# Kernel tuning notes

Measured on AMD Instinct MI355X. Metric: run time of the kernel, lower is better.

## Reference

```python
import jax, jax.numpy as jnp
import numpy as np
from functools import partial

D_MODEL = 256
D_STATE = 16
DT_RANK = 16  # ceil(d_model/16)
LN_EPS = 1e-5


def setup_inputs() -> dict:
    key = jax.random.key(0)
    ks = jax.random.split(key, 8)
    B, L, d, N, r = 16, 2048, D_MODEL, D_STATE, DT_RANK
    x = jax.random.normal(ks[0], (B, L, d), dtype=jnp.float32)
    # LayerNorm params
    ln_w = jnp.ones((d,), jnp.float32)
    ln_b = jnp.zeros((d,), jnp.float32)
    # S6 params
    x_proj_w = jax.random.normal(ks[1], (d, r + 2 * N), jnp.float32) / np.sqrt(d)
    dt_proj_w = jax.random.normal(ks[2], (r, d), jnp.float32) / np.sqrt(r)
    dt_proj_b = jax.random.uniform(ks[3], (d,), jnp.float32, -4.0, -2.0)  # softplus -> small dt
    A_log = jnp.log(jnp.tile(jnp.arange(1, N + 1, dtype=jnp.float32), (d, 1)))  # (d, N)
    D_skip = jnp.ones((d,), jnp.float32)
    # GLU params
    glu_w = jax.random.normal(ks[4], (d, 2 * d), jnp.float32) / np.sqrt(d)
    glu_b = jnp.zeros((2 * d,), jnp.float32)
    return {"x": x, "ln_w": ln_w, "ln_b": ln_b, "x_proj_w": x_proj_w,
            "dt_proj_w": dt_proj_w, "dt_proj_b": dt_proj_b, "A_log": A_log,
            "D_skip": D_skip, "glu_w": glu_w, "glu_b": glu_b}


def _layernorm(x, w, b):
    mu = jnp.mean(x, -1, keepdims=True)
    var = jnp.mean(jnp.square(x - mu), -1, keepdims=True)
    return (x - mu) * jax.lax.rsqrt(var + LN_EPS) * w + b


def _s6(x, x_proj_w, dt_proj_w, dt_proj_b, A_log, D_skip):
    # x: (B, L, d) selective scan (S6)
    Bsz, L, d = x.shape
    N = A_log.shape[1]
    A = -jnp.exp(A_log)                       # (d, N)
    dbl = x @ x_proj_w                        # (B, L, r+2N)
    dt, Bm, Cm = jnp.split(dbl, [DT_RANK, DT_RANK + N], axis=-1)
    delta = jax.nn.softplus(dt @ dt_proj_w + dt_proj_b)  # (B, L, d)

    def step(h, inp):
        d_t, b_t, c_t, x_t = inp              # (B,d),(B,N),(B,N),(B,d)
        dA = jnp.exp(d_t[..., None] * A)      # (B, d, N)
        h = dA * h + (d_t * x_t)[..., None] * b_t[:, None, :]
        y = jnp.einsum('bdn,bn->bd', h, c_t)
        return h, y

    h0 = jnp.zeros((Bsz, d, N), x.dtype)
    xs = (jnp.swapaxes(delta, 0, 1), jnp.swapaxes(Bm, 0, 1),
          jnp.swapaxes(Cm, 0, 1), jnp.swapaxes(x, 0, 1))
    _, ys = jax.lax.scan(step, h0, xs)        # ys: (L, B, d)
    return jnp.swapaxes(ys, 0, 1) + x * D_skip


def _glu(x, w, b):
    d = x.shape[-1]
    out = x @ w + b
    return out[..., :d] * jax.nn.sigmoid(out[..., d:])


@jax.jit
def reference(x, ln_w, ln_b, x_proj_w, dt_proj_w, dt_proj_b, A_log, D_skip, glu_w, glu_b):
    skip = x
    h = _layernorm(x, ln_w, ln_b)
    h = _s6(h, x_proj_w, dt_proj_w, dt_proj_b, A_log, D_skip)
    h = jax.nn.gelu(h, approximate=False)     # dropout = identity (eval)
    h = _glu(h, glu_w, glu_b)
    return h + skip
```

## Files before the change

### kernel.cpp

```cpp
#include <hip/hip_runtime.h>
#include <hip/hip_bf16.h>

#define BB 16
#define LL 2048
#define DD 256
#define NN 16
#define RR 16
#define CH 64
#define LC (LL/CH)

static __device__ __forceinline__ float bf2f(unsigned short u) {
    return __uint_as_float(((unsigned)u) << 16);
}
static __device__ __forceinline__ unsigned short f2bf(float f) {
    unsigned u = __float_as_uint(f);
    u += 0x7FFFu + ((u >> 16) & 1u);
    return (unsigned short)(u >> 16);
}

typedef __attribute__((ext_vector_type(8))) short bf16x8;
typedef __attribute__((ext_vector_type(4))) short bf16x4;
typedef __attribute__((ext_vector_type(4))) float f32x4;

static __device__ __forceinline__ void pow_tree(float E, float* e) {
    e[0] = E;
    e[1] = E * E;
    e[2] = e[1] * E;
    e[3] = e[1] * e[1];
    e[4] = e[3] * e[0];  e[5] = e[3] * e[1];  e[6] = e[3] * e[2];  e[7] = e[3] * e[3];
    e[8] = e[7] * e[0];  e[9] = e[7] * e[1];  e[10] = e[7] * e[2]; e[11] = e[7] * e[3];
    e[12] = e[7] * e[4]; e[13] = e[7] * e[5]; e[14] = e[7] * e[6]; e[15] = e[7] * e[7];
}

__global__ __launch_bounds__(256) void k_prep_wx(
    const float* __restrict__ xw, unsigned short* __restrict__ Wxt)
{
    const int idx = blockIdx.x * 256 + threadIdx.x;
    const int n  = idx >> 6;
    const int k0 = (idx & 63) * 4;
    #pragma unroll
    for (int i = 0; i < 4; ++i) {
        float v = (n < 48) ? xw[(size_t)(k0 + i) * 48 + n] : 0.f;
        Wxt[(size_t)n * DD + k0 + i] = f2bf(v);
    }
}

__global__ __launch_bounds__(256) void k_transpose(
    const float* __restrict__ W, unsigned short* __restrict__ Wt)
{
    __shared__ unsigned short s[32][33];
    const int bx = blockIdx.x;
    const int by = blockIdx.y;
    const int t = threadIdx.x;
    const int r = t >> 5, cc = t & 31;
    #pragma unroll
    for (int i = 0; i < 4; ++i)
        s[r + 8*i][cc] = f2bf(W[(size_t)(by*32 + r + 8*i)*512 + bx*32 + cc]);
    __syncthreads();
    #pragma unroll
    for (int i = 0; i < 4; ++i)
        Wt[(size_t)(bx*32 + r + 8*i)*256 + by*32 + cc] = s[cc][r + 8*i];
}

template<bool FAST>
__device__ __forceinline__ void dt_scan1(
    const float (*sdt)[20], const unsigned short (*As)[264],
    const float (*sB)[16], const float* wj, float bia,
    const float* al, int d, size_t m0,
    unsigned short* __restrict__ delta,
    float* h, float* dsum)
{
    #pragma unroll 4
    for (int l = 0; l < LC; ++l) {
        float acc = bia;
        #pragma unroll
        for (int j = 0; j < 16; ++j)
            acc = fmaf(sdt[l][j], wj[j], acc);
        const float sp = (acc > 15.f) ? acc
            : 0.69314718f * log2f(1.f + exp2f(acc * 1.44269504f));
        const unsigned short dbits = f2bf(sp);
        delta[(m0 + l)*DD + d] = dbits;
        const float dl = bf2f(dbits);
        const float xl = bf2f(As[l][d]);
        const float dx = dl * xl;
        *dsum += dl;
        float e[NN];
        if (FAST) pow_tree(exp2f(al[0]*dl), e);
        else {
            #pragma unroll
            for (int n = 0; n < NN; ++n) e[n] = exp2f(al[n]*dl);
        }
        #pragma unroll
        for (int n = 0; n < NN; ++n)
            h[n] = fmaf(e[n], h[n], dx * sB[l][n]);
    }
}

__global__ __launch_bounds__(256) void k_ln_scan1(
    const float* __restrict__ x,
    const float* __restrict__ ln_w,
    const float* __restrict__ ln_b,
    const unsigned short* __restrict__ Wxt,
    const float* __restrict__ dtw,
    const float* __restrict__ dtb,
    const float* __restrict__ A_log,
    unsigned short* __restrict__ xln,
    unsigned short* __restrict__ delta,
    float* __restrict__ Bv,
    float* __restrict__ Cv,
    float* __restrict__ S,
    float* __restrict__ Dsum)
{
    const int t = threadIdx.x;
    const int blk = blockIdx.x;
    const size_t m0 = (size_t)blk * 32;
    const int row = t >> 3, seg = t & 7;
    const size_t grow = m0 + row;

    __shared__ unsigned short As[32][264];
    __shared__ float sdt[32][20];
    __shared__ float sB[32][16];
    __shared__ float slnw[256], slnb[256], sdtb[256];

    {
        const int tt = t & 63;
        if (t < 64)       *(float4*)&slnw[tt*4] = *(const float4*)&ln_w[tt*4];
        else if (t < 128) *(float4*)&slnb[tt*4] = *(const float4*)&ln_b[tt*4];
        else if (t < 192) *(float4*)&sdtb[tt*4] = *(const float4*)&dtb[tt*4];
    }

    float wj[16];
    #pragma unroll
    for (int j = 0; j < 16; ++j) wj[j] = dtw[j*DD + t];
    float al[NN];
    bool fast = true;
    #pragma unroll
    for (int n = 0; n < NN; ++n) {
        al[n] = -expf(A_log[t*NN + n]) * 1.44269504f;
        fast = fast && (fabsf(al[n] - (n+1)*al[0]) <= 1e-3f*fabsf(al[n]) + 1e-6f);
    }

    float v[32];
    #pragma unroll
    for (int i = 0; i < 8; ++i)
        *(float4*)&v[i*4] = *(const float4*)(x + grow*DD + i*32 + seg*4);
    float s = 0.f, q = 0.f;
    #pragma unroll
    for (int i = 0; i < 32; ++i) { s += v[i]; q = fmaf(v[i], v[i], q); }
    #pragma unroll
    for (int o = 1; o < 8; o <<= 1) {
        s += __shfl_xor(s, o);
        q += __shfl_xor(q, o);
    }
    const float mu = s * (1.f/DD);
    const float rs = rsqrtf(q * (1.f/DD) - mu*mu + 1e-5f);
    __syncthreads();

    #pragma unroll
    for (int i = 0; i < 8; ++i) {
        const int c = i*32 + seg*4;
        const float4 wv = *(const float4*)&slnw[c];
        const float4 bv = *(const float4*)&slnb[c];
        unsigned short o16[4];
        o16[0] = f2bf((v[i*4+0]-mu)*rs*wv.x + bv.x);
        o16[1] = f2bf((v[i*4+1]-mu)*rs*wv.y + bv.y);
        o16[2] = f2bf((v[i*4+2]-mu)*rs*wv.z + bv.z);
        o16[3] = f2bf((v[i*4+3]-mu)*rs*wv.w + bv.w);
        *(bf16x4*)&xln[grow*DD + c] = *(bf16x4*)&o16[0];
        *(bf16x4*)&As[row][c]       = *(bf16x4*)&o16[0];
    }
    __syncthreads();

    {
        const int w = t >> 6, lane = t & 63;
        const int cl = lane & 15, rq = lane >> 4;
        const int mh = (w & 1) * 16;
        const int nh = (w >> 1) * 32;
        f32x4 acc0 = {0.f,0.f,0.f,0.f}, acc1 = {0.f,0.f,0.f,0.f};
        #pragma unroll
        for (int k0 = 0; k0 < 256; k0 += 32) {
            const bf16x8 a  = *(const bf16x8*)&As[mh + cl][k0 + rq*8];
            const bf16x8 b0 = *(const bf16x8*)&Wxt[(size_t)(nh + cl)*DD + k0 + rq*8];
            acc0 = __builtin_amdgcn_mfma_f32_16x16x32_bf16(a, b0, acc0, 0, 0, 0);
            if (w < 2) {
                const bf16x8 b1 = *(const bf16x8*)&Wxt[(size_t)(nh + 16 + cl)*DD + k0 + rq*8];
                acc1 = __builtin_amdgcn_mfma_f32_16x16x32_bf16(a, b1, acc1, 0, 0, 0);
            }
        }
        if (w < 2) {
            #pragma unroll
            for (int r = 0; r < 4; ++r) {
                const int rr = mh + rq*4 + r;
                sdt[rr][cl] = acc0[r];
                sB[rr][cl]  = acc1[r];
                Bv[(m0 + rr)*NN + cl] = acc1[r];
            }
        } else {
            #pragma unroll
            for (int r = 0; r < 4; ++r)
                Cv[(m0 + mh + rq*4 + r)*NN + cl] = acc0[r];
        }
    }
    __syncthreads();

    float h[NN];
    #pragma unroll
    for (int n = 0; n < NN; ++n) h[n] = 0.f;
    float dsum = 0.f;
    const float bia = sdtb[t];
    if (fast) dt_scan1<true >(sdt, As, sB, wj, bia, al, t, m0, delta, h, &dsum);
    else      dt_scan1<false>(sdt, As, sB, wj, bia, al, t, m0, delta, h, &dsum);
    const size_t o = (size_t)blk * NN * DD + t;
    #pragma unroll
    for (int n = 0; n < NN; ++n) S[o + n*DD] = h[n];
    Dsum[(size_t)blk*DD + t] = dsum;
}

__global__ __launch_bounds__(256) void k_combine(
    const float* __restrict__ S, const float* __restrict__ Dsum,
    const float* __restrict__ A_log, float* __restrict__ Hin)
{
    const int bi = blockIdx.x;
    const int d = threadIdx.x;
    const int n = bi & 15;
    const int b = bi >> 4;
    const float al = -expf(A_log[d*NN + n]) * 1.44269504f;
    float h = 0.f;
    for (int c0 = 0; c0 < CH; c0 += 8) {
        float ds8[8], s8[8];
        #pragma unroll
        for (int i = 0; i < 8; ++i) {
            const size_t blk = (size_t)b*CH + c0 + i;
            ds8[i] = Dsum[blk*DD + d];
            s8[i]  = S[(blk*NN + n)*DD + d];
        }
        #pragma unroll
        for (int i = 0; i < 8; ++i) {
            const size_t blk = (size_t)b*CH + c0 + i;
            Hin[(blk*NN + n)*DD + d] = h;
            h = fmaf(exp2f(al * ds8[i]), h, s8[i]);
        }
    }
}

template<bool FAST>
__device__ __forceinline__ void scan2_impl(
    const unsigned short (*sD)[264], const unsigned short (*sX)[264],
    const float (*sB)[16], const float (*sC)[16],
    const float* al, int d, float* h, float dsk,
    size_t gout, unsigned short* __restrict__ g)
{
    #pragma unroll 4
    for (int l = 0; l < LC; ++l) {
        const float dl = bf2f(sD[l][d]);
        const float xl = bf2f(sX[l][d]);
        const float dx = dl * xl;
        float e[NN];
        if (FAST) pow_tree(exp2f(al[0]*dl), e);
        else {
            #pragma unroll
            for (int n = 0; n < NN; ++n) e[n] = exp2f(al[n]*dl);
        }
        float yb[4] = {0.f, 0.f, 0.f, 0.f};
        #pragma unroll
        for (int n = 0; n < NN; ++n) {
            h[n] = fmaf(e[n], h[n], dx * sB[l][n]);
            yb[n & 3] = fmaf(h[n], sC[l][n], yb[n & 3]);
        }
        const float vv = (yb[0]+yb[1]) + (yb[2]+yb[3]) + xl * dsk;
        const float u  = 0.7978845608f * (vv + 0.044715f*vv*vv*vv);
        const float t2 = exp2f(2.8853900818f * u);
        const float th = 1.f - 2.f/(t2 + 1.f);
        g[gout + (size_t)l*DD] = f2bf(0.5f * vv * (1.f + th));
    }
}

__global__ __launch_bounds__(256) void k_scan2(
    const unsigned short* __restrict__ delta,
    const unsigned short* __restrict__ xln,
    const float* __restrict__ Bv,
    const float* __restrict__ Cv,
    const float* __restrict__ A_log,
    const float* __restrict__ Hin,
    const float* __restrict__ Dskip,
    unsigned short* __restrict__ g)
{
    const int blk = blockIdx.x;
    const int c = blk & (CH-1);
    const int b = blk >> 6;
    const int d = threadIdx.x;
    const int l0 = c * LC;
    __shared__ unsigned short sD[LC][264];
    __shared__ unsigned short sX[LC][264];
    __shared__ float sB[LC][16], sC[LC][16];

    {
        const int sr = d >> 3, sc = (d & 7) * 32;
        const size_t gbase = ((size_t)b*LL + l0 + sr)*DD + sc;
        #pragma unroll
        for (int i = 0; i < 4; ++i) {
            *(bf16x8*)&sD[sr][sc + i*8] = *(const bf16x8*)&delta[gbase + i*8];
            *(bf16x8*)&sX[sr][sc + i*8] = *(const bf16x8*)&xln  [gbase + i*8];
        }
        if (d < 128) {
            const int l = d >> 2, qq = (d & 3) * 4;
            *(float4*)&sB[l][qq] = *(const float4*)&Bv[((size_t)b*LL + l0 + l)*NN + qq];
        } else {
            const int dd = d - 128;
            const int l = dd >> 2, qq = (dd & 3) * 4;
            *(float4*)&sC[l][qq] = *(const float4*)&Cv[((size_t)b*LL + l0 + l)*NN + qq];
        }
    }
    float al[NN];
    bool fast = true;
    #pragma unroll
    for (int n = 0; n < NN; ++n) {
        al[n] = -expf(A_log[d*NN + n]) * 1.44269504f;
        fast = fast && (fabsf(al[n] - (n+1)*al[0]) <= 1e-3f*fabsf(al[n]) + 1e-6f);
    }
    float h[NN];
    const size_t ob = (size_t)blk * NN * DD + d;
    #pragma unroll
    for (int n = 0; n < NN; ++n) h[n] = Hin[ob + n*DD];
    const float dsk = Dskip[d];
    __syncthreads();
    const size_t gout = ((size_t)b*LL + l0)*DD + d;
    if (fast) scan2_impl<true >(sD, sX, sB, sC, al, d, h, dsk, gout, g);
    else      scan2_impl<false>(sD, sX, sB, sC, al, d, h, dsk, gout, g);
}

__global__ __launch_bounds__(256) void k_glu(
    const unsigned short* __restrict__ g,
    const unsigned short* __restrict__ Wt,
    const float* __restrict__ gb,
    const float* __restrict__ x,
    float* __restrict__ out)
{
    __shared__ unsigned short As[64][40];
    __shared__ unsigned short Bl[64][40];
    __shared__ unsigned short Bh[64][40];
    const int n0 = blockIdx.x * 64;
    const int m0 = blockIdx.y * 64;
    const int t = threadIdx.x;
    const int w = t >> 6, lane = t & 63;
    const int r = t >> 2, q = t & 3;
    const int cl = lane & 15, rq = lane >> 4;
    f32x4 accL[4], accH[4];
    const f32x4 zz = {0.f, 0.f, 0.f, 0.f};
    #pragma unroll
    for (int nf = 0; nf < 4; ++nf) { accL[nf] = zz; accH[nf] = zz; }

    for (int k0 = 0; k0 < 256; k0 += 32) {
        *(bf16x8*)(&As[r][q*8]) = *(const bf16x8*)(&g [(size_t)(m0+r)*DD + k0 + q*8]);
        *(bf16x8*)(&Bl[r][q*8]) = *(const bf16x8*)(&Wt[(size_t)(n0+r)*DD + k0 + q*8]);
        *(bf16x8*)(&Bh[r][q*8]) = *(const bf16x8*)(&Wt[(size_t)(n0+256+r)*DD + k0 + q*8]);
        __syncthreads();
        const bf16x8 a = *(const bf16x8*)(&As[w*16 + cl][rq*8]);
        #pragma unroll
        for (int nf = 0; nf < 4; ++nf) {
            const bf16x8 bl = *(const bf16x8*)(&Bl[nf*16 + cl][rq*8]);
            const bf16x8 bh = *(const bf16x8*)(&Bh[nf*16 + cl][rq*8]);
            accL[nf] = __builtin_amdgcn_mfma_f32_16x16x32_bf16(a, bl, accL[nf], 0, 0, 0);
            accH[nf] = __builtin_amdgcn_mfma_f32_16x16x32_bf16(a, bh, accH[nf], 0, 0, 0);
        }
        __syncthreads();
    }
    #pragma unroll
    for (int nf = 0; nf < 4; ++nf) {
        const int j = n0 + nf*16 + cl;
        const float bL = gb[j];
        const float bH = gb[j + 256];
        #pragma unroll
        for (int rr = 0; rr < 4; ++rr) {
            const int m = m0 + w*16 + rq*4 + rr;
            const float lo = accL[nf][rr] + bL;
            const float hi = accH[nf][rr] + bH;
            const float sg = 1.f / (1.f + exp2f(-1.44269504f * hi));
            out[(size_t)m*DD + j] = lo * sg + x[(size_t)m*DD + j];
        }
    }
}

extern "C" void kernel_launch(void* const* d_in, const int* in_sizes, int n_in,
                              void* d_out, int out_size, void* d_ws, size_t ws_size,
                              hipStream_t stream)
{
    const float* x    = (const float*)d_in[0];
    const float* ln_w = (const float*)d_in[1];
    const float* ln_b = (const float*)d_in[2];
    const float* xpw  = (const float*)d_in[3];
    const float* dtw  = (const float*)d_in[4];
    const float* dtb  = (const float*)d_in[5];
    const float* alog = (const float*)d_in[6];
    const float* dsk  = (const float*)d_in[7];
    const float* gw   = (const float*)d_in[8];
    const float* gb   = (const float*)d_in[9];
    float* out = (float*)d_out;

    char* ws = (char*)d_ws;
    size_t off = 0;
    auto alloc = [&](size_t bytes) {
        char* p = ws + off; off += (bytes + 255) & ~(size_t)255; return p;
    };
    unsigned short* xln   = (unsigned short*)alloc((size_t)BB*LL*DD*2);
    unsigned short* delta = (unsigned short*)alloc((size_t)BB*LL*DD*2);
    float*          Bvp   = (float*)         alloc((size_t)BB*LL*NN*4);
    float*          Cvp   = (float*)         alloc((size_t)BB*LL*NN*4);
    float*          S     = (float*)         alloc((size_t)BB*CH*NN*DD*4);
    float*          Dsum  = (float*)         alloc((size_t)BB*CH*DD*4);
    float*          Hin   = (float*)         alloc((size_t)BB*CH*NN*DD*4);
    unsigned short* Wt    = (unsigned short*)alloc((size_t)512*256*2);
    unsigned short* Wxt   = (unsigned short*)alloc((size_t)64*256*2);
    unsigned short* g     = delta;

    k_prep_wx<<<16, 256, 0, stream>>>(xpw, Wxt);
    k_transpose<<<dim3(16, 8), 256, 0, stream>>>(gw, Wt);
    k_ln_scan1<<<BB*CH, 256, 0, stream>>>(x, ln_w, ln_b, Wxt, dtw, dtb, alog,
                                          xln, delta, Bvp, Cvp, S, Dsum);
    k_combine<<<256, 256, 0, stream>>>(S, Dsum, alog, Hin);
    k_scan2<<<BB*CH, 256, 0, stream>>>(delta, xln, Bvp, Cvp, alog, Hin, dsk, g);
    k_glu<<<dim3(4, 512), 256, 0, stream>>>(g, Wt, gb, x, out);
}
```

Before: 116.6 us.

## Fuse LayerNorm, chunked scan, combine and scan2 into one persistent kernel with grid barriers

Replaces the three-kernel chunked scan with one persistent kernel of 512 blocks that keeps the LayerNorm output, dt, B and C in shared memory. It uses software grid barriers between the chunk-local scan, the cross-chunk combine and the second scan. This removes the global round trips for xln, delta, B and C plus two kernel launches, at the cost of recomputing the dt projection and softplus in the second pass. It also merges the two weight-prep kernels into one launch. The fused path runs only when the occupancy query says all blocks can be resident; otherwise it falls back to the old kernels.

```diff
diff --git a/kernel.cpp b/kernel.cpp
--- a/kernel.cpp
+++ b/kernel.cpp
@@ -6,8 +6,10 @@
 #define DD 256
 #define NN 16
 #define RR 16
-#define CH 64
-#define LC (LL/CH)
+#define CHF 32
+#define LCF 64
+#define CHB 64
+#define LCB 32
 
 static __device__ __forceinline__ float bf2f(unsigned short u) {
     return __uint_as_float(((unsigned)u) << 16);
@@ -32,38 +34,277 @@
     e[12] = e[7] * e[4]; e[13] = e[7] * e[5]; e[14] = e[7] * e[6]; e[15] = e[7] * e[7];
 }
 
-__global__ __launch_bounds__(256) void k_prep_wx(
-    const float* __restrict__ xw, unsigned short* __restrict__ Wxt)
-{
-    const int idx = blockIdx.x * 256 + threadIdx.x;
-    const int n  = idx >> 6;
-    const int k0 = (idx & 63) * 4;
-    #pragma unroll
-    for (int i = 0; i < 4; ++i) {
-        float v = (n < 48) ? xw[(size_t)(k0 + i) * 48 + n] : 0.f;
-        Wxt[(size_t)n * DD + k0 + i] = f2bf(v);
-    }
-}
-
-__global__ __launch_bounds__(256) void k_transpose(
-    const float* __restrict__ W, unsigned short* __restrict__ Wt)
+static __device__ __forceinline__ void gridBarrier(unsigned* bar, unsigned nblk) {
+    __threadfence();
+    __syncthreads();
+    if (threadIdx.x == 0) {
+        unsigned* cnt = bar;
+        unsigned* gen = bar + 32;
+        const unsigned gsnap = atomicAdd(gen, 0u);
+        const unsigned arrived = atomicAdd(cnt, 1u) + 1u;
+        if (arrived == nblk) {
+            atomicExch(cnt, 0u);
+            __threadfence();
+            atomicAdd(gen, 1u);
+        } else {
+            while (atomicAdd(gen, 0u) == gsnap)
+                __builtin_amdgcn_s_sleep(2);
+        }
+    }
+    __syncthreads();
+    __threadfence();
+}
+
+__global__ __launch_bounds__(256) void k_prep(
+    const float* __restrict__ xw, const float* __restrict__ gw,
+    unsigned short* __restrict__ Wxt, unsigned short* __restrict__ Wt)
 {
     __shared__ unsigned short s[32][33];
-    const int bx = blockIdx.x;
-    const int by = blockIdx.y;
+    const int bid = blockIdx.x;
     const int t = threadIdx.x;
-    const int r = t >> 5, cc = t & 31;
-    #pragma unroll
-    for (int i = 0; i < 4; ++i)
-        s[r + 8*i][cc] = f2bf(W[(size_t)(by*32 + r + 8*i)*512 + bx*32 + cc]);
-    __syncthreads();
-    #pragma unroll
-    for (int i = 0; i < 4; ++i)
-        Wt[(size_t)(bx*32 + r + 8*i)*256 + by*32 + cc] = s[cc][r + 8*i];
+    if (bid < 16) {
+        const int idx = bid * 256 + t;
+        const int n  = idx >> 6;
+        const int k0 = (idx & 63) * 4;
+        #pragma unroll
+        for (int i = 0; i < 4; ++i) {
+            float v = (n < 48) ? xw[(size_t)(k0 + i) * 48 + n] : 0.f;
+            Wxt[(size_t)n * DD + k0 + i] = f2bf(v);
+        }
+    } else {
+        const int bb = bid - 16;
+        const int bx = bb & 15, by = bb >> 4;
+        const int r = t >> 5, cc = t & 31;
+        #pragma unroll
+        for (int i = 0; i < 4; ++i)
+            s[r + 8*i][cc] = f2bf(gw[(size_t)(by*32 + r + 8*i)*512 + bx*32 + cc]);
+        __syncthreads();
+        #pragma unroll
+        for (int i = 0; i < 4; ++i)
+            Wt[(size_t)(bx*32 + r + 8*i)*256 + by*32 + cc] = s[cc][r + 8*i];
+    }
 }
 
 template<bool FAST>
-__device__ __forceinline__ void dt_scan1(
+__device__ __forceinline__ void fused_scan1(
+    const float (*sdt)[20], const unsigned short (*As)[264],
+    const float (*sB)[17], const float* wj, float bia,
+    const float* al, int t, float* h, float* dsum)
+{
+    #pragma unroll 4
+    for (int l = 0; l < LCF; ++l) {
+        float acc = bia;
+        #pragma unroll
+        for (int j = 0; j < 16; ++j)
+            acc = fmaf(sdt[l][j], wj[j], acc);
+        const float sp = (acc > 15.f) ? acc
+            : 0.69314718f * log2f(1.f + exp2f(acc * 1.44269504f));
+        const float dl = bf2f(f2bf(sp));
+        const float xl = bf2f(As[l][t]);
+        const float dx = dl * xl;
+        *dsum += dl;
+        float e[NN];
+        if (FAST) pow_tree(exp2f(al[0]*dl), e);
+        else {
+            #pragma unroll
+            for (int n = 0; n < NN; ++n) e[n] = exp2f(al[n]*dl);
+        }
+        #pragma unroll
+        for (int n = 0; n < NN; ++n)
+            h[n] = fmaf(e[n], h[n], dx * sB[l][n]);
+    }
+}
+
+template<bool FAST>
+__device__ __forceinline__ void fused_scan2(
+    const float (*sdt)[20], const unsigned short (*As)[264],
+    const float (*sB)[17], const float (*sC)[17],
+    const float* wj, float bia, const float* al, int t,
+    float* h, float dsk, size_t m0, unsigned short* __restrict__ g)
+{
+    #pragma unroll 4
+    for (int l = 0; l < LCF; ++l) {
+        float acc = bia;
+        #pragma unroll
+        for (int j = 0; j < 16; ++j)
+            acc = fmaf(sdt[l][j], wj[j], acc);
+        const float sp = (acc > 15.f) ? acc
+            : 0.69314718f * log2f(1.f + exp2f(acc * 1.44269504f));
+        const float dl = bf2f(f2bf(sp));
+        const float xl = bf2f(As[l][t]);
+        const float dx = dl * xl;
+        float e[NN];
+        if (FAST) pow_tree(exp2f(al[0]*dl), e);
+        else {
+            #pragma unroll
+            for (int n = 0; n < NN; ++n) e[n] = exp2f(al[n]*dl);
+        }
+        float yb[4] = {0.f, 0.f, 0.f, 0.f};
+        #pragma unroll
+        for (int n = 0; n < NN; ++n) {
+            h[n] = fmaf(e[n], h[n], dx * sB[l][n]);
+            yb[n & 3] = fmaf(h[n], sC[l][n], yb[n & 3]);
+        }
+        const float vv = (yb[0]+yb[1]) + (yb[2]+yb[3]) + xl * dsk;
+        const float u  = 0.7978845608f * (vv + 0.044715f*vv*vv*vv);
+        const float t2 = exp2f(2.8853900818f * u);
+        const float th = 1.f - 2.f/(t2 + 1.f);
+        g[(m0 + l)*DD + t] = f2bf(0.5f * vv * (1.f + th));
+    }
+}
+
+__global__ __launch_bounds__(256) void k_fused(
+    const float* __restrict__ x,
+    const float* __restrict__ ln_w,
+    const float* __restrict__ ln_b,
+    const unsigned short* __restrict__ Wxt,
+    const float* __restrict__ dtw,
+    const float* __restrict__ dtb,
+    const float* __restrict__ A_log,
+    const float* __restrict__ Dskip,
+    float* __restrict__ S,
+    float* __restrict__ Dsum,
+    float* __restrict__ Hin,
+    unsigned short* __restrict__ g,
+    unsigned* __restrict__ bar)
+{
+    const int t = threadIdx.x;
+    const int blk = blockIdx.x;
+    const size_t m0 = (size_t)blk * LCF;
+
+    __shared__ unsigned short As[LCF][264];
+    __shared__ float sdt[LCF][20];
+    __shared__ float sB[LCF][17];
+    __shared__ float sC[LCF][17];
+    __shared__ float slnw[256], slnb[256], sdtb[256];
+
+    {
+        const int tt = t & 63;
+        if (t < 64)       *(float4*)&slnw[tt*4] = *(const float4*)&ln_w[tt*4];
+        else if (t < 128) *(float4*)&slnb[tt*4] = *(const float4*)&ln_b[tt*4];
+        else if (t < 192) *(float4*)&sdtb[tt*4] = *(const float4*)&dtb[tt*4];
+    }
+
+    float wj[16];
+    #pragma unroll
+    for (int j = 0; j < 16; ++j) wj[j] = dtw[j*DD + t];
+    float al[NN];
+    bool fast = true;
+    #pragma unroll
+    for (int n = 0; n < NN; ++n) {
+        al[n] = -expf(A_log[t*NN + n]) * 1.44269504f;
+        fast = fast && (fabsf(al[n] - (n+1)*al[0]) <= 1e-3f*fabsf(al[n]) + 1e-6f);
+    }
+    const float dsk = Dskip[t];
+    __syncthreads();
+
+    const int seg = t & 7;
+    #pragma unroll
+    for (int half = 0; half < 2; ++half) {
+        const int row = (t >> 3) + 32*half;
+        const size_t grow = m0 + row;
+        float v[32];
+        #pragma unroll
+        for (int i = 0; i < 8; ++i)
+            *(float4*)&v[i*4] = *(const float4*)(x + grow*DD + i*32 + seg*4);
+        float s = 0.f, q = 0.f;
+        #pragma unroll
+        for (int i = 0; i < 32; ++i) { s += v[i]; q = fmaf(v[i], v[i], q); }
+        #pragma unroll
+        for (int o = 1; o < 8; o <<= 1) {
+            s += __shfl_xor(s, o);
+            q += __shfl_xor(q, o);
+        }
+        const float mu = s * (1.f/DD);
+        const float rs = rsqrtf(q * (1.f/DD) - mu*mu + 1e-5f);
+        #pragma unroll
+        for (int i = 0; i < 8; ++i) {
+            const int c = i*32 + seg*4;
+            const float4 wv = *(const float4*)&slnw[c];
+            const float4 bv = *(const float4*)&slnb[c];
+            unsigned short o16[4];
+            o16[0] = f2bf((v[i*4+0]-mu)*rs*wv.x + bv.x);
+            o16[1] = f2bf((v[i*4+1]-mu)*rs*wv.y + bv.y);
+            o16[2] = f2bf((v[i*4+2]-mu)*rs*wv.z + bv.z);
+            o16[3] = f2bf((v[i*4+3]-mu)*rs*wv.w + bv.w);
+            *(bf16x4*)&As[row][c] = *(bf16x4*)&o16[0];
+        }
+    }
+    __syncthreads();
+
+    {
+        const int w = t >> 6, lane = t & 63;
+        const int cl = lane & 15, rq = lane >> 4;
+        const int mrow = w * 16;
+        f32x4 aDt = {0.f,0.f,0.f,0.f}, aB = {0.f,0.f,0.f,0.f}, aC = {0.f,0.f,0.f,0.f};
+        #pragma unroll
+        for (int k0 = 0; k0 < 256; k0 += 32) {
+            const bf16x8 a  = *(const bf16x8*)&As[mrow + cl][k0 + rq*8];
+            const bf16x8 b0 = *(const bf16x8*)&Wxt[(size_t)(cl)*DD      + k0 + rq*8];
+            const bf16x8 b1 = *(const bf16x8*)&Wxt[(size_t)(16+cl)*DD   + k0 + rq*8];
+            const bf16x8 b2 = *(const bf16x8*)&Wxt[(size_t)(32+cl)*DD   + k0 + rq*8];
+            aDt = __builtin_amdgcn_mfma_f32_16x16x32_bf16(a, b0, aDt, 0, 0, 0);
+            aB  = __builtin_amdgcn_mfma_f32_16x16x32_bf16(a, b1, aB,  0, 0, 0);
+            aC  = __builtin_amdgcn_mfma_f32_16x16x32_bf16(a, b2, aC,  0, 0, 0);
+        }
+        #pragma unroll
+        for (int r = 0; r < 4; ++r) {
+            const int rr = mrow + rq*4 + r;
+            sdt[rr][cl] = aDt[r];
+            sB[rr][cl]  = aB[r];
+            sC[rr][cl]  = aC[r];
+        }
+    }
+    __syncthreads();
+
+    float h[NN];
+    #pragma unroll
+    for (int n = 0; n < NN; ++n) h[n] = 0.f;
+    float dsum = 0.f;
+    const float bia = sdtb[t];
+    if (fast) fused_scan1<true >(sdt, As, sB, wj, bia, al, t, h, &dsum);
+    else      fused_scan1<false>(sdt, As, sB, wj, bia, al, t, h, &dsum);
+    {
+        const size_t o = (size_t)blk * NN * DD + t;
+        #pragma unroll
+        for (int n = 0; n < NN; ++n) S[o + n*DD] = h[n];
+        Dsum[(size_t)blk*DD + t] = dsum;
+    }
+    gridBarrier(bar, BB*CHF);
+
+    if (blk < 256) {
+        const int n2 = blk & 15, b2 = blk >> 4;
+        const float al2 = -expf(A_log[t*NN + n2]) * 1.44269504f;
+        float hh = 0.f;
+        for (int c0 = 0; c0 < CHF; c0 += 16) {
+            float ds16[16], s16[16];
+            #pragma unroll
+            for (int i = 0; i < 16; ++i) {
+                const size_t bc = (size_t)b2*CHF + c0 + i;
+                ds16[i] = Dsum[bc*DD + t];
+                s16[i]  = S[(bc*NN + n2)*DD + t];
+            }
+            #pragma unroll
+            for (int i = 0; i < 16; ++i) {
+                const size_t bc = (size_t)b2*CHF + c0 + i;
+                Hin[(bc*NN + n2)*DD + t] = hh;
+                hh = fmaf(exp2f(al2 * ds16[i]), hh, s16[i]);
+            }
+        }
+    }
+    gridBarrier(bar, BB*CHF);
+
+    {
+        const size_t ob = (size_t)blk * NN * DD + t;
+        #pragma unroll
+        for (int n = 0; n < NN; ++n) h[n] = Hin[ob + n*DD];
+    }
+    if (fast) fused_scan2<true >(sdt, As, sB, sC, wj, bia, al, t, h, dsk, m0, g);
+    else      fused_scan2<false>(sdt, As, sB, sC, wj, bia, al, t, h, dsk, m0, g);
+}
+
+template<bool FAST>
+__device__ __forceinline__ void dt_scan1_fb(
     const float (*sdt)[20], const unsigned short (*As)[264],
     const float (*sB)[16], const float* wj, float bia,
     const float* al, int d, size_t m0,
@@ -71,7 +312,7 @@
     float* h, float* dsum)
 {
     #pragma unroll 4
-    for (int l = 0; l < LC; ++l) {
+    for (int l = 0; l < LCB; ++l) {
         float acc = bia;
         #pragma unroll
         for (int j = 0; j < 16; ++j)
@@ -128,7 +369,6 @@
         else if (t < 128) *(float4*)&slnb[tt*4] = *(const float4*)&ln_b[tt*4];
         else if (t < 192) *(float4*)&sdtb[tt*4] = *(const float4*)&dtb[tt*4];
     }
-
     float wj[16];
     #pragma unroll
     for (int j = 0; j < 16; ++j) wj[j] = dtw[j*DD + t];
@@ -139,7 +379,6 @@
         al[n] = -expf(A_log[t*NN + n]) * 1.44269504f;
         fast = fast && (fabsf(al[n] - (n+1)*al[0]) <= 1e-3f*fabsf(al[n]) + 1e-6f);
     }
-
     float v[32];
     #pragma unroll
     for (int i = 0; i < 8; ++i)
@@ -155,7 +394,6 @@
     const float mu = s * (1.f/DD);
     const float rs = rsqrtf(q * (1.f/DD) - mu*mu + 1e-5f);
     __syncthreads();
-
     #pragma unroll
     for (int i = 0; i < 8; ++i) {
         const int c = i*32 + seg*4;
@@ -170,7 +408,6 @@
         *(bf16x4*)&As[row][c]       = *(bf16x4*)&o16[0];
     }
     __syncthreads();
-
     {
         const int w = t >> 6, lane = t & 63;
         const int cl = lane & 15, rq = lane >> 4;
@@ -202,14 +439,13 @@
         }
     }
     __syncthreads();
-
     float h[NN];
     #pragma unroll
     for (int n = 0; n < NN; ++n) h[n] = 0.f;
     float dsum = 0.f;
     const float bia = sdtb[t];
-    if (fast) dt_scan1<true >(sdt, As, sB, wj, bia, al, t, m0, delta, h, &dsum);
-    else      dt_scan1<false>(sdt, As, sB, wj, bia, al, t, m0, delta, h, &dsum);
+    if (fast) dt_scan1_fb<true >(sdt, As, sB, wj, bia, al, t, m0, delta, h, &dsum);
+    else      dt_scan1_fb<false>(sdt, As, sB, wj, bia, al, t, m0, delta, h, &dsum);
     const size_t o = (size_t)blk * NN * DD + t;
     #pragma unroll
     for (int n = 0; n < NN; ++n) S[o + n*DD] = h[n];
@@ -226,17 +462,17 @@
     const int b = bi >> 4;
     const float al = -expf(A_log[d*NN + n]) * 1.44269504f;
     float h = 0.f;
-    for (int c0 = 0; c0 < CH; c0 += 8) {
+    for (int c0 = 0; c0 < CHB; c0 += 8) {
         float ds8[8], s8[8];
         #pragma unroll
         for (int i = 0; i < 8; ++i) {
-            const size_t blk = (size_t)b*CH + c0 + i;
+            const size_t blk = (size_t)b*CHB + c0 + i;
             ds8[i] = Dsum[blk*DD + d];
             s8[i]  = S[(blk*NN + n)*DD + d];
         }
         #pragma unroll
         for (int i = 0; i < 8; ++i) {
-            const size_t blk = (size_t)b*CH + c0 + i;
+            const size_t blk = (size_t)b*CHB + c0 + i;
             Hin[(blk*NN + n)*DD + d] = h;
             h = fmaf(exp2f(al * ds8[i]), h, s8[i]);
         }
@@ -244,14 +480,14 @@
 }
 
 template<bool FAST>
-__device__ __forceinline__ void scan2_impl(
+__device__ __forceinline__ void scan2_impl_fb(
     const unsigned short (*sD)[264], const unsigned short (*sX)[264],
     const float (*sB)[16], const float (*sC)[16],
     const float* al, int d, float* h, float dsk,
     size_t gout, unsigned short* __restrict__ g)
 {
     #pragma unroll 4
-    for (int l = 0; l < LC; ++l) {
+    for (int l = 0; l < LCB; ++l) {
         const float dl = bf2f(sD[l][d]);
         const float xl = bf2f(sX[l][d]);
         const float dx = dl * xl;
@@ -286,14 +522,13 @@
     unsigned short* __restrict__ g)
 {
     const int blk = blockIdx.x;
-    const int c = blk & (CH-1);
+    const int c = blk & (CHB-1);
     const int b = blk >> 6;
     const int d = threadIdx.x;
-    const int l0 = c * LC;
-    __shared__ unsigned short sD[LC][264];
-    __shared__ unsigned short sX[LC][264];
-    __shared__ float sB[LC][16], sC[LC][16];
-
+    const int l0 = c * LCB;
+    __shared__ unsigned short sD[LCB][264];
+    __shared__ unsigned short sX[LCB][264];
+    __shared__ float sB[LCB][16], sC[LCB][16];
     {
         const int sr = d >> 3, sc = (d & 7) * 32;
         const size_t gbase = ((size_t)b*LL + l0 + sr)*DD + sc;
@@ -325,8 +560,8 @@
     const float dsk = Dskip[d];
     __syncthreads();
     const size_t gout = ((size_t)b*LL + l0)*DD + d;
-    if (fast) scan2_impl<true >(sD, sX, sB, sC, al, d, h, dsk, gout, g);
-    else      scan2_impl<false>(sD, sX, sB, sC, al, d, h, dsk, gout, g);
+    if (fast) scan2_impl_fb<true >(sD, sX, sB, sC, al, d, h, dsk, gout, g);
+    else      scan2_impl_fb<false>(sD, sX, sB, sC, al, d, h, dsk, gout, g);
 }
 
 __global__ __launch_bounds__(256) void k_glu(
@@ -402,22 +637,37 @@
     auto alloc = [&](size_t bytes) {
         char* p = ws + off; off += (bytes + 255) & ~(size_t)255; return p;
     };
-    unsigned short* xln   = (unsigned short*)alloc((size_t)BB*LL*DD*2);
-    unsigned short* delta = (unsigned short*)alloc((size_t)BB*LL*DD*2);
-    float*          Bvp   = (float*)         alloc((size_t)BB*LL*NN*4);
-    float*          Cvp   = (float*)         alloc((size_t)BB*LL*NN*4);
-    float*          S     = (float*)         alloc((size_t)BB*CH*NN*DD*4);
-    float*          Dsum  = (float*)         alloc((size_t)BB*CH*DD*4);
-    float*          Hin   = (float*)         alloc((size_t)BB*CH*NN*DD*4);
-    unsigned short* Wt    = (unsigned short*)alloc((size_t)512*256*2);
-    unsigned short* Wxt   = (unsigned short*)alloc((size_t)64*256*2);
-    unsigned short* g     = delta;
-
-    k_prep_wx<<<16, 256, 0, stream>>>(xpw, Wxt);
-    k_transpose<<<dim3(16, 8), 256, 0, stream>>>(gw, Wt);
-    k_ln_scan1<<<BB*CH, 256, 0, stream>>>(x, ln_w, ln_b, Wxt, dtw, dtb, alog,
-                                          xln, delta, Bvp, Cvp, S, Dsum);
-    k_combine<<<256, 256, 0, stream>>>(S, Dsum, alog, Hin);
-    k_scan2<<<BB*CH, 256, 0, stream>>>(delta, xln, Bvp, Cvp, alog, Hin, dsk, g);
+    unsigned*       bar    = (unsigned*)      alloc(256);
+    unsigned short* xln    = (unsigned short*)alloc((size_t)BB*LL*DD*2);
+    unsigned short* deltaG = (unsigned short*)alloc((size_t)BB*LL*DD*2);
+    float*          Bvp    = (float*)         alloc((size_t)BB*LL*NN*4);
+    float*          Cvp    = (float*)         alloc((size_t)BB*LL*NN*4);
+    float*          S      = (float*)         alloc((size_t)BB*CHB*NN*DD*4);
+    float*          Dsum   = (float*)         alloc((size_t)BB*CHB*DD*4);
+    float*          Hin    = (float*)         alloc((size_t)BB*CHB*NN*DD*4);
+    unsigned short* Wt     = (unsigned short*)alloc((size_t)512*256*2);
+    unsigned short* Wxt    = (unsigned short*)alloc((size_t)64*256*2);
+    unsigned short* g      = deltaG;
+
+    k_prep<<<144, 256, 0, stream>>>(xpw, gw, Wxt, Wt);
+
+    int occ = 0, ncu = 0, dev = 0;
+    bool coop = false;
+    if (hipGetDevice(&dev) == hipSuccess &&
+        hipOccupancyMaxActiveBlocksPerMultiprocessor(&occ, k_fused, 256, 0) == hipSuccess &&
+        hipDeviceGetAttribute(&ncu, hipDeviceAttributeMultiprocessorCount, dev) == hipSuccess)
+        coop = (occ * ncu >= BB*CHF);
+
+    if (coop) {
+        hipMemsetAsync(bar, 0, 256, stream);
+        k_fused<<<BB*CHF, 256, 0, stream>>>(x, ln_w, ln_b, Wxt, dtw, dtb, alog,
+                                            dsk, S, Dsum, Hin, g, bar);
+    } else {
+        k_ln_scan1<<<BB*CHB, 256, 0, stream>>>(x, ln_w, ln_b, Wxt, dtw, dtb, alog,
+                                               xln, deltaG, Bvp, Cvp, S, Dsum);
+        k_combine<<<256, 256, 0, stream>>>(S, Dsum, alog, Hin);
+        k_scan2<<<BB*CHB, 256, 0, stream>>>(deltaG, xln, Bvp, Cvp, alog, Hin, dsk, g);
+    }
+
     k_glu<<<dim3(4, 512), 256, 0, stream>>>(g, Wt, gb, x, out);
 }
```

Result: faster. 110.1 us (-5.6%).

## Compute dt projection with MFMA before scan and merge weight prep kernels

Applied to the files above, without the earlier changes.

Moves the per-step 16-wide dt projection out of the serial scan loop in k_ln_scan1. It is replaced by a block-wide bf16 MFMA pass that writes softplus(delta) into shared memory and global memory before the scan starts. The two weight-prep kernels are merged into a single launch that also emits a padded bf16 transposed dt_proj weight. B and C shared rows are padded to 20 floats and read as float4 vectors in both scans. In exchange, the dt projection input is now rounded to bf16, a precision loss, and the kernel gains an extra sync and more shared memory.

```diff
diff --git a/kernel.cpp b/kernel.cpp
--- a/kernel.cpp
+++ b/kernel.cpp
@@ -32,56 +32,57 @@
     e[12] = e[7] * e[4]; e[13] = e[7] * e[5]; e[14] = e[7] * e[6]; e[15] = e[7] * e[7];
 }
 
-__global__ __launch_bounds__(256) void k_prep_wx(
-    const float* __restrict__ xw, unsigned short* __restrict__ Wxt)
-{
-    const int idx = blockIdx.x * 256 + threadIdx.x;
-    const int n  = idx >> 6;
-    const int k0 = (idx & 63) * 4;
-    #pragma unroll
-    for (int i = 0; i < 4; ++i) {
-        float v = (n < 48) ? xw[(size_t)(k0 + i) * 48 + n] : 0.f;
-        Wxt[(size_t)n * DD + k0 + i] = f2bf(v);
-    }
-}
-
-__global__ __launch_bounds__(256) void k_transpose(
-    const float* __restrict__ W, unsigned short* __restrict__ Wt)
+__global__ __launch_bounds__(256) void k_prep(
+    const float* __restrict__ xw, const float* __restrict__ gw,
+    const float* __restrict__ dtw,
+    unsigned short* __restrict__ Wxt, unsigned short* __restrict__ Wt,
+    unsigned short* __restrict__ Dwt)
 {
     __shared__ unsigned short s[32][33];
-    const int bx = blockIdx.x;
-    const int by = blockIdx.y;
+    const int bid = blockIdx.x;
     const int t = threadIdx.x;
-    const int r = t >> 5, cc = t & 31;
-    #pragma unroll
-    for (int i = 0; i < 4; ++i)
-        s[r + 8*i][cc] = f2bf(W[(size_t)(by*32 + r + 8*i)*512 + bx*32 + cc]);
-    __syncthreads();
-    #pragma unroll
-    for (int i = 0; i < 4; ++i)
-        Wt[(size_t)(bx*32 + r + 8*i)*256 + by*32 + cc] = s[cc][r + 8*i];
+    if (bid < 16) {
+        const int idx = bid * 256 + t;
+        const int n  = idx >> 6;
+        const int k0 = (idx & 63) * 4;
+        #pragma unroll
+        for (int i = 0; i < 4; ++i) {
+            float v = (n < 48) ? xw[(size_t)(k0 + i) * 48 + n] : 0.f;
+            Wxt[(size_t)n * DD + k0 + i] = f2bf(v);
+        }
+    } else if (bid < 144) {
+        const int bb = bid - 16;
+        const int bx = bb & 15, by = bb >> 4;
+        const int r = t >> 5, cc = t & 31;
+        #pragma unroll
+        for (int i = 0; i < 4; ++i)
+            s[r + 8*i][cc] = f2bf(gw[(size_t)(by*32 + r + 8*i)*512 + bx*32 + cc]);
+        __syncthreads();
+        #pragma unroll
+        for (int i = 0; i < 4; ++i)
+            Wt[(size_t)(bx*32 + r + 8*i)*256 + by*32 + cc] = s[cc][r + 8*i];
+    } else {
+        unsigned short r32[32];
+        #pragma unroll
+        for (int k = 0; k < 16; ++k) r32[k] = f2bf(dtw[(size_t)k*DD + t]);
+        #pragma unroll
+        for (int k = 16; k < 32; ++k) r32[k] = 0;
+        #pragma unroll
+        for (int i = 0; i < 4; ++i)
+            *(bf16x8*)&Dwt[(size_t)t*32 + i*8] = *(bf16x8*)&r32[i*8];
+    }
 }
 
 template<bool FAST>
-__device__ __forceinline__ void dt_scan1(
-    const float (*sdt)[20], const unsigned short (*As)[264],
-    const float (*sB)[16], const float* wj, float bia,
-    const float* al, int d, size_t m0,
-    unsigned short* __restrict__ delta,
+__device__ __forceinline__ void scan1_loop(
+    const unsigned short (*sDel)[264], const unsigned short (*As)[264],
+    const float (*sB)[20], const float* al, int t,
     float* h, float* dsum)
 {
     #pragma unroll 4
     for (int l = 0; l < LC; ++l) {
-        float acc = bia;
-        #pragma unroll
-        for (int j = 0; j < 16; ++j)
-            acc = fmaf(sdt[l][j], wj[j], acc);
-        const float sp = (acc > 15.f) ? acc
-            : 0.69314718f * log2f(1.f + exp2f(acc * 1.44269504f));
-        const unsigned short dbits = f2bf(sp);
-        delta[(m0 + l)*DD + d] = dbits;
-        const float dl = bf2f(dbits);
-        const float xl = bf2f(As[l][d]);
+        const float dl = bf2f(sDel[l][t]);
+        const float xl = bf2f(As[l][t]);
         const float dx = dl * xl;
         *dsum += dl;
         float e[NN];
@@ -90,9 +91,15 @@
             #pragma unroll
             for (int n = 0; n < NN; ++n) e[n] = exp2f(al[n]*dl);
         }
+        const float4 B0 = *(const float4*)&sB[l][0];
+        const float4 B1 = *(const float4*)&sB[l][4];
+        const float4 B2 = *(const float4*)&sB[l][8];
+        const float4 B3 = *(const float4*)&sB[l][12];
+        const float bb[16] = {B0.x,B0.y,B0.z,B0.w, B1.x,B1.y,B1.z,B1.w,
+                              B2.x,B2.y,B2.z,B2.w, B3.x,B3.y,B3.z,B3.w};
         #pragma unroll
         for (int n = 0; n < NN; ++n)
-            h[n] = fmaf(e[n], h[n], dx * sB[l][n]);
+            h[n] = fmaf(e[n], h[n], dx * bb[n]);
     }
 }
 
@@ -101,7 +108,7 @@
     const float* __restrict__ ln_w,
     const float* __restrict__ ln_b,
     const unsigned short* __restrict__ Wxt,
-    const float* __restrict__ dtw,
+    const unsigned short* __restrict__ Dwt,
     const float* __restrict__ dtb,
     const float* __restrict__ A_log,
     unsigned short* __restrict__ xln,
@@ -113,13 +120,14 @@
 {
     const int t = threadIdx.x;
     const int blk = blockIdx.x;
-    const size_t m0 = (size_t)blk * 32;
+    const size_t m0 = (size_t)blk * LC;
     const int row = t >> 3, seg = t & 7;
     const size_t grow = m0 + row;
 
-    __shared__ unsigned short As[32][264];
-    __shared__ float sdt[32][20];
-    __shared__ float sB[32][16];
+    __shared__ unsigned short As[LC][264];
+    __shared__ unsigned short sDel[LC][264];
+    __shared__ unsigned short sdt16[LC][40];
+    __shared__ float sB[LC][20];
     __shared__ float slnw[256], slnb[256], sdtb[256];
 
     {
@@ -127,11 +135,11 @@
         if (t < 64)       *(float4*)&slnw[tt*4] = *(const float4*)&ln_w[tt*4];
         else if (t < 128) *(float4*)&slnb[tt*4] = *(const float4*)&ln_b[tt*4];
         else if (t < 192) *(float4*)&sdtb[tt*4] = *(const float4*)&dtb[tt*4];
-    }
-
-    float wj[16];
-    #pragma unroll
-    for (int j = 0; j < 16; ++j) wj[j] = dtw[j*DD + t];
+        if (t < 64) {
+            const bf16x8 z = {0,0,0,0,0,0,0,0};
+            *(bf16x8*)&sdt16[t >> 1][16 + (t & 1)*8] = z;
+        }
+    }
     float al[NN];
     bool fast = true;
     #pragma unroll
@@ -155,7 +163,6 @@
     const float mu = s * (1.f/DD);
     const float rs = rsqrtf(q * (1.f/DD) - mu*mu + 1e-5f);
     __syncthreads();
-
     #pragma unroll
     for (int i = 0; i < 8; ++i) {
         const int c = i*32 + seg*4;
@@ -171,9 +178,10 @@
     }
     __syncthreads();
 
+    const int w = t >> 6, lane = t & 63;
+    const int cl = lane & 15, rq = lane >> 4;
+
     {
-        const int w = t >> 6, lane = t & 63;
-        const int cl = lane & 15, rq = lane >> 4;
         const int mh = (w & 1) * 16;
         const int nh = (w >> 1) * 32;
         f32x4 acc0 = {0.f,0.f,0.f,0.f}, acc1 = {0.f,0.f,0.f,0.f};
@@ -191,8 +199,8 @@
             #pragma unroll
             for (int r = 0; r < 4; ++r) {
                 const int rr = mh + rq*4 + r;
-                sdt[rr][cl] = acc0[r];
-                sB[rr][cl]  = acc1[r];
+                sdt16[rr][cl] = f2bf(acc0[r]);
+                sB[rr][cl]    = acc1[r];
                 Bv[(m0 + rr)*NN + cl] = acc1[r];
             }
         } else {
@@ -203,13 +211,37 @@
     }
     __syncthreads();
 
+    {
+        const int mh = (w & 1) * 16;
+        const int nbase = (w >> 1) * 8;
+        const bf16x8 a = *(const bf16x8*)&sdt16[mh + cl][rq*8];
+        #pragma unroll
+        for (int nt = 0; nt < 8; ++nt) {
+            const int n0 = (nbase + nt) * 16;
+            const bf16x8 b = *(const bf16x8*)&Dwt[(size_t)(n0 + cl)*32 + rq*8];
+            f32x4 acc = {0.f,0.f,0.f,0.f};
+            acc = __builtin_amdgcn_mfma_f32_16x16x32_bf16(a, b, acc, 0, 0, 0);
+            const float bia = sdtb[n0 + cl];
+            #pragma unroll
+            for (int r = 0; r < 4; ++r) {
+                const float ac = acc[r] + bia;
+                const float sp = (ac > 15.f) ? ac
+                    : 0.69314718f * log2f(1.f + exp2f(ac * 1.44269504f));
+                const unsigned short db = f2bf(sp);
+                const int rr = mh + rq*4 + r;
+                sDel[rr][n0 + cl] = db;
+                delta[(m0 + rr)*DD + n0 + cl] = db;
+            }
+        }
+    }
+    __syncthreads();
+
     float h[NN];
     #pragma unroll
     for (int n = 0; n < NN; ++n) h[n] = 0.f;
     float dsum = 0.f;
-    const float bia = sdtb[t];
-    if (fast) dt_scan1<true >(sdt, As, sB, wj, bia, al, t, m0, delta, h, &dsum);
-    else      dt_scan1<false>(sdt, As, sB, wj, bia, al, t, m0, delta, h, &dsum);
+    if (fast) scan1_loop<true >(sDel, As, sB, al, t, h, &dsum);
+    else      scan1_loop<false>(sDel, As, sB, al, t, h, &dsum);
     const size_t o = (size_t)blk * NN * DD + t;
     #pragma unroll
     for (int n = 0; n < NN; ++n) S[o + n*DD] = h[n];
@@ -244,9 +276,9 @@
 }
 
 template<bool FAST>
-__device__ __forceinline__ void scan2_impl(
+__device__ __forceinline__ void scan2_loop(
     const unsigned short (*sD)[264], const unsigned short (*sX)[264],
-    const float (*sB)[16], const float (*sC)[16],
+    const float (*sB)[20], const float (*sC)[20],
     const float* al, int d, float* h, float dsk,
     size_t gout, unsigned short* __restrict__ g)
 {
@@ -261,11 +293,23 @@
             #pragma unroll
             for (int n = 0; n < NN; ++n) e[n] = exp2f(al[n]*dl);
         }
+        const float4 B0 = *(const float4*)&sB[l][0];
+        const float4 B1 = *(const float4*)&sB[l][4];
+        const float4 B2 = *(const float4*)&sB[l][8];
+        const float4 B3 = *(const float4*)&sB[l][12];
+        const float bb[16] = {B0.x,B0.y,B0.z,B0.w, B1.x,B1.y,B1.z,B1.w,
+                              B2.x,B2.y,B2.z,B2.w, B3.x,B3.y,B3.z,B3.w};
+        const float4 C0 = *(const float4*)&sC[l][0];
+        const float4 C1 = *(const float4*)&sC[l][4];
+        const float4 C2 = *(const float4*)&sC[l][8];
+        const float4 C3 = *(const float4*)&sC[l][12];
+        const float cc[16] = {C0.x,C0.y,C0.z,C0.w, C1.x,C1.y,C1.z,C1.w,
+                              C2.x,C2.y,C2.z,C2.w, C3.x,C3.y,C3.z,C3.w};
         float yb[4] = {0.f, 0.f, 0.f, 0.f};
         #pragma unroll
         for (int n = 0; n < NN; ++n) {
-            h[n] = fmaf(e[n], h[n], dx * sB[l][n]);
-            yb[n & 3] = fmaf(h[n], sC[l][n], yb[n & 3]);
+            h[n] = fmaf(e[n], h[n], dx * bb[n]);
+            yb[n & 3] = fmaf(h[n], cc[n], yb[n & 3]);
         }
         const float vv = (yb[0]+yb[1]) + (yb[2]+yb[3]) + xl * dsk;
         const float u  = 0.7978845608f * (vv + 0.044715f*vv*vv*vv);
@@ -292,8 +336,7 @@
     const int l0 = c * LC;
     __shared__ unsigned short sD[LC][264];
     __shared__ unsigned short sX[LC][264];
-    __shared__ float sB[LC][16], sC[LC][16];
-
+    __shared__ float sB[LC][20], sC[LC][20];
     {
         const int sr = d >> 3, sc = (d & 7) * 32;
         const size_t gbase = ((size_t)b*LL + l0 + sr)*DD + sc;
@@ -325,8 +368,8 @@
     const float dsk = Dskip[d];
     __syncthreads();
     const size_t gout = ((size_t)b*LL + l0)*DD + d;
-    if (fast) scan2_impl<true >(sD, sX, sB, sC, al, d, h, dsk, gout, g);
-    else      scan2_impl<false>(sD, sX, sB, sC, al, d, h, dsk, gout, g);
+    if (fast) scan2_loop<true >(sD, sX, sB, sC, al, d, h, dsk, gout, g);
+    else      scan2_loop<false>(sD, sX, sB, sC, al, d, h, dsk, gout, g);
 }
 
 __global__ __launch_bounds__(256) void k_glu(
@@ -402,22 +445,22 @@
     auto alloc = [&](size_t bytes) {
         char* p = ws + off; off += (bytes + 255) & ~(size_t)255; return p;
     };
-    unsigned short* xln   = (unsigned short*)alloc((size_t)BB*LL*DD*2);
-    unsigned short* delta = (unsigned short*)alloc((size_t)BB*LL*DD*2);
-    float*          Bvp   = (float*)         alloc((size_t)BB*LL*NN*4);
-    float*          Cvp   = (float*)         alloc((size_t)BB*LL*NN*4);
-    float*          S     = (float*)         alloc((size_t)BB*CH*NN*DD*4);
-    float*          Dsum  = (float*)         alloc((size_t)BB*CH*DD*4);
-    float*          Hin   = (float*)         alloc((size_t)BB*CH*NN*DD*4);
-    unsigned short* Wt    = (unsigned short*)alloc((size_t)512*256*2);
-    unsigned short* Wxt   = (unsigned short*)alloc((size_t)64*256*2);
-    unsigned short* g     = delta;
-
-    k_prep_wx<<<16, 256, 0, stream>>>(xpw, Wxt);
-    k_transpose<<<dim3(16, 8), 256, 0, stream>>>(gw, Wt);
-    k_ln_scan1<<<BB*CH, 256, 0, stream>>>(x, ln_w, ln_b, Wxt, dtw, dtb, alog,
-                                          xln, delta, Bvp, Cvp, S, Dsum);
+    unsigned short* xln    = (unsigned short*)alloc((size_t)BB*LL*DD*2);
+    unsigned short* deltaG = (unsigned short*)alloc((size_t)BB*LL*DD*2);
+    float*          Bvp    = (float*)         alloc((size_t)BB*LL*NN*4);
+    float*          Cvp    = (float*)         alloc((size_t)BB*LL*NN*4);
+    float*          S      = (float*)         alloc((size_t)BB*CH*NN*DD*4);
+    float*          Dsum   = (float*)         alloc((size_t)BB*CH*DD*4);
+    float*          Hin    = (float*)         alloc((size_t)BB*CH*NN*DD*4);
+    unsigned short* Wt     = (unsigned short*)alloc((size_t)512*256*2);
+    unsigned short* Wxt    = (unsigned short*)alloc((size_t)64*256*2);
+    unsigned short* Dwt    = (unsigned short*)alloc((size_t)256*32*2);
+    unsigned short* g      = deltaG;
+
+    k_prep<<<145, 256, 0, stream>>>(xpw, gw, dtw, Wxt, Wt, Dwt);
+    k_ln_scan1<<<BB*CH, 256, 0, stream>>>(x, ln_w, ln_b, Wxt, Dwt, dtb, alog,
+                                          xln, deltaG, Bvp, Cvp, S, Dsum);
     k_combine<<<256, 256, 0, stream>>>(S, Dsum, alog, Hin);
-    k_scan2<<<BB*CH, 256, 0, stream>>>(delta, xln, Bvp, Cvp, alog, Hin, dsk, g);
+    k_scan2<<<BB*CH, 256, 0, stream>>>(deltaG, xln, Bvp, Cvp, alog, Hin, dsk, g);
     k_glu<<<dim3(4, 512), 256, 0, stream>>>(g, Wt, gb, x, out);
 }
```

Result: faster. 113.2 us (-3.0%).
